# Optimization experiments

Measured on AMD Instinct MI355X. Metric: run time of the kernel, lower is better.

## Reference

```python
import jax, jax.numpy as jnp
import numpy as np

N = 2048            # num nodes
AVG_DEG = 16
E0 = N * AVG_DEG    # random edges; self-loops appended -> E = E0 + N
IN_FEATS = 256
H = 16              # num_heads
HS = 32             # hidden_size (forced by linear001 = Linear(32,16))
D = HS // H         # head_dim = 2
EPS = 1e-5


def gat_conv(x, src, dst, W, al, ar, b):
    # DGL-style GATConv: x [N,F] -> [N,H,D]
    feat = (x @ W).reshape(N, H, D)                      # [N,H,D]
    el = (feat * al[None]).sum(-1)                       # [N,H] (src term)
    er = (feat * ar[None]).sum(-1)                       # [N,H] (dst term)
    e = jax.nn.leaky_relu(el[src] + er[dst], 0.2)        # [E,H]
    m = jax.ops.segment_max(e, dst, num_segments=N)      # segment softmax over incoming edges
    ex = jnp.exp(e - m[dst])
    s = jax.ops.segment_sum(ex, dst, num_segments=N)
    alpha = ex / s[dst]                                  # [E,H]
    out = jax.ops.segment_sum(alpha[:, :, None] * feat[src], dst, num_segments=N)
    return out + b.reshape(1, H, D)


def setup_inputs() -> dict:
    key = jax.random.key(0)
    ks = jax.random.split(key, 40)
    rn = lambda k, s, sc=0.1: (jax.random.normal(k, s, jnp.float32) * sc)
    loops = jnp.arange(N, dtype=jnp.int32)
    src = jnp.concatenate([jax.random.randint(ks[0], (E0,), 0, N, jnp.int32), loops])
    dst = jnp.concatenate([jax.random.randint(ks[1], (E0,), 0, N, jnp.int32), loops])
    inp = {
        'features': jax.random.normal(ks[2], (N, IN_FEATS), jnp.float32),
        'src': src, 'dst': dst,
        # GATConv 1
        'W1': rn(ks[3], (IN_FEATS, HS)), 'al1': rn(ks[4], (H, D)), 'ar1': rn(ks[5], (H, D)), 'bg1': rn(ks[6], (HS,)),
        # GATConv 2
        'W2': rn(ks[7], (HS, HS)), 'al2': rn(ks[8], (H, D)), 'ar2': rn(ks[9], (H, D)), 'bg2': rn(ks[10], (HS,)),
        # dense MHA projections
        'qw': rn(ks[11], (HS, HS)), 'qb': rn(ks[12], (HS,)),
        'kw': rn(ks[13], (HS, HS)), 'kb': rn(ks[14], (HS,)),
        'vw': rn(ks[15], (HS, HS)), 'vb': rn(ks[16], (HS,)),
        'ow': rn(ks[17], (HS, HS)), 'ob': rn(ks[18], (HS,)),
        # batchnorm affine
        'bn_g': jnp.ones((HS,), jnp.float32), 'bn_b': jnp.zeros((HS,), jnp.float32),
        # mlp
        'm1w': rn(ks[19], (HS, HS // 2)), 'm1b': rn(ks[20], (HS // 2,)),
        'm2w': rn(ks[21], (HS // 2, HS)), 'm2b': rn(ks[22], (HS,)),
        # scoring head
        'w001': rn(ks[23], (32, 16)), 'b001': rn(ks[24], (16,)),
        'w01': rn(ks[25], (16, 8)), 'b01': rn(ks[26], (8,)),
        'w1': rn(ks[27], (8, 4)), 'b1': rn(ks[28], (4,)),
        'w2': rn(ks[29], (4, 1)), 'b2': rn(ks[30], (1,)),
    }
    return inp


def reference(features, src, dst, W1, al1, ar1, bg1, W2, al2, ar2, bg2,
              qw, qb, kw, kb, vw, vb, ow, ob, bn_g, bn_b,
              m1w, m1b, m2w, m2b, w001, b001, w01, b01, w1, b1, w2, b2):
    h = gat_conv(features, src, dst, W1, al1, ar1, bg1).reshape(N, HS)
    h = gat_conv(h, src, dst, W2, al2, ar2, bg2).reshape(N, HS)
    # manual dense multi-head attention across all nodes
    Q = (h @ qw + qb).reshape(N, H, D)
    K = (h @ kw + kb).reshape(N, H, D)
    V = (h @ vw + vb).reshape(N, H, D)
    scores = jnp.einsum('nhd,mhd->hnm', Q, K) / jnp.sqrt(jnp.float32(D))  # [H,N,N]
    attn = jax.nn.softmax(scores, axis=-1)
    ao = jnp.einsum('hnm,mhd->nhd', attn, V).reshape(N, HS)
    ao = ao @ ow + ob
    # BatchNorm1d (training mode: batch stats, biased variance)
    mu = ao.mean(0)
    var = ao.var(0)
    ao = (ao - mu) / jnp.sqrt(var + EPS) * bn_g + bn_b
    # MLP
    ao = jax.nn.relu(ao @ m1w + m1b)
    ao = jax.nn.relu(ao @ m2w + m2b)
    # scoring head
    z = jax.nn.leaky_relu(ao @ w001 + b001, 0.01)
    z = jax.nn.leaky_relu(z @ w01 + b01, 0.01)
    z = jax.nn.leaky_relu(z @ w1 + b1, 0.01)
    return jax.nn.sigmoid(z @ w2 + b2)  # [N,1]
```

## Files before the change

### kernel.cpp

```cpp
#include <hip/hip_runtime.h>
#include <math.h>

#define NN 2048
#define NH 16
#define HSZ 32
#define INF_ 256
#define CAP 64

__global__ void __launch_bounds__(256) k_front(
    const float* __restrict__ x, const float* __restrict__ W1,
    const float* __restrict__ al, const float* __restrict__ ar,
    const int* __restrict__ src, const int* __restrict__ dst, int E,
    int* __restrict__ cnt, int* __restrict__ adj, float* __restrict__ feat,
    float* __restrict__ el, float* __restrict__ er) {
    __shared__ float xs[4][INF_];
    __shared__ float row[4][HSZ];
    const int tid = threadIdx.x;
    const int gtid = blockIdx.x * 256 + tid;
    const int lane = tid & 63, wsl = tid >> 6, gw = gtid >> 6;
    const int j = lane & 31, half = lane >> 5;

    if (gtid < E) {
        int d = dst[gtid];
        int pos = atomicAdd(&cnt[d], 1);
        if (pos < CAP) adj[d * CAP + pos] = src[gtid];
    }

    int n = gw;
    ((float4*)xs[wsl])[lane] = ((const float4*)(x + (size_t)n * INF_))[lane];
    __syncthreads();
    float acc = 0.f;
    const float4* x4 = (const float4*)xs[wsl];
#pragma unroll
    for (int k4 = 0; k4 < 32; ++k4) {
        float4 xq = x4[half * 32 + k4];
        int k = half * 128 + 4 * k4;
        acc += xq.x * W1[(k + 0) * HSZ + j];
        acc += xq.y * W1[(k + 1) * HSZ + j];
        acc += xq.z * W1[(k + 2) * HSZ + j];
        acc += xq.w * W1[(k + 3) * HSZ + j];
    }
    acc += __shfl_xor(acc, 32);
    if (half == 0) {
        feat[n * HSZ + j] = acc;
        row[wsl][j] = acc;
    }
    __syncthreads();
    if (lane < NH) {
        el[n * NH + lane] =
            row[wsl][2 * lane] * al[2 * lane] + row[wsl][2 * lane + 1] * al[2 * lane + 1];
    } else if (lane < 2 * NH) {
        int h = lane - NH;
        er[n * NH + h] =
            row[wsl][2 * h] * ar[2 * h] + row[wsl][2 * h + 1] * ar[2 * h + 1];
    }
}

__global__ void __launch_bounds__(256) k_seg_gat2(
    const int* __restrict__ cnt, const int* __restrict__ adj,
    const float* __restrict__ el, const float* __restrict__ er,
    const float* __restrict__ feat, const float* __restrict__ bg,
    const float* __restrict__ W2, const float* __restrict__ al2,
    const float* __restrict__ ar2, float* __restrict__ feat2,
    float* __restrict__ el2, float* __restrict__ er2) {
    __shared__ float row[4][HSZ];
    __shared__ float xv[4][HSZ];
    const int tid = threadIdx.x;
    const int gtid = blockIdx.x * 256 + tid;
    const int lane = tid & 63, wsl = tid >> 6, gw = gtid >> 6;
    const int j = lane & 31, half = lane >> 5;
    int n = gw;
    int h = lane >> 2, q = lane & 3;
    int deg = cnt[n]; deg = deg < CAP ? deg : CAP;
    int base = n * CAP;
    float erv = er[n * NH + h];
    float sum = 0.f, a0 = 0.f, a1 = 0.f;
    for (int jj = q; jj < deg; jj += 4) {
        int s = adj[base + jj];
        float v = el[s * NH + h] + erv;
        v = v > 0.f ? v : 0.2f * v;
        float ex = __expf(v);
        float2 f = ((const float2*)feat)[s * NH + h];
        sum += ex; a0 += ex * f.x; a1 += ex * f.y;
    }
    sum += __shfl_xor(sum, 1); a0 += __shfl_xor(a0, 1); a1 += __shfl_xor(a1, 1);
    sum += __shfl_xor(sum, 2); a0 += __shfl_xor(a0, 2); a1 += __shfl_xor(a1, 2);
    if (q == 0) {
        float rs = 1.f / sum;
        row[wsl][2 * h]     = a0 * rs + bg[2 * h];
        row[wsl][2 * h + 1] = a1 * rs + bg[2 * h + 1];
    }
    __syncthreads();
    float acc = 0.f;
#pragma unroll
    for (int c = half * 16; c < half * 16 + 16; ++c) acc += row[wsl][c] * W2[c * HSZ + j];
    acc += __shfl_xor(acc, 32);
    if (half == 0) {
        feat2[n * HSZ + j] = acc;
        xv[wsl][j] = acc;
    }
    __syncthreads();
    if (lane < NH) {
        el2[n * NH + lane] =
            xv[wsl][2 * lane] * al2[2 * lane] + xv[wsl][2 * lane + 1] * al2[2 * lane + 1];
    } else if (lane < 2 * NH) {
        int h2 = lane - NH;
        er2[n * NH + h2] =
            xv[wsl][2 * h2] * ar2[2 * h2] + xv[wsl][2 * h2 + 1] * ar2[2 * h2 + 1];
    }
}

__global__ void __launch_bounds__(256) k_seg_qkv(
    const int* __restrict__ cnt, const int* __restrict__ adj,
    const float* __restrict__ el2, const float* __restrict__ er2,
    const float* __restrict__ feat2, const float* __restrict__ bg,
    const float* __restrict__ qw, const float* __restrict__ qb,
    const float* __restrict__ kw, const float* __restrict__ kb,
    const float* __restrict__ vw, const float* __restrict__ vb,
    float* __restrict__ Q, float* __restrict__ KV) {
    __shared__ float row[4][HSZ];
    const int tid = threadIdx.x;
    const int gtid = blockIdx.x * 256 + tid;
    const int lane = tid & 63, wsl = tid >> 6, gw = gtid >> 6;
    const int j = lane & 31, half = lane >> 5;
    int n = gw;
    int h = lane >> 2, q = lane & 3;
    int deg = cnt[n]; deg = deg < CAP ? deg : CAP;
    int base = n * CAP;
    float erv = er2[n * NH + h];
    float sum = 0.f, a0 = 0.f, a1 = 0.f;
    for (int jj = q; jj < deg; jj += 4) {
        int s = adj[base + jj];
        float v = el2[s * NH + h] + erv;
        v = v > 0.f ? v : 0.2f * v;
        float ex = __expf(v);
        float2 f = ((const float2*)feat2)[s * NH + h];
        sum += ex; a0 += ex * f.x; a1 += ex * f.y;
    }
    sum += __shfl_xor(sum, 1); a0 += __shfl_xor(a0, 1); a1 += __shfl_xor(a1, 1);
    sum += __shfl_xor(sum, 2); a0 += __shfl_xor(a0, 2); a1 += __shfl_xor(a1, 2);
    if (q == 0) {
        float rs = 1.f / sum;
        row[wsl][2 * h]     = a0 * rs + bg[2 * h];
        row[wsl][2 * h + 1] = a1 * rs + bg[2 * h + 1];
    }
    __syncthreads();
    float qa = 0.f, ka = 0.f, va = 0.f;
#pragma unroll
    for (int c = half * 16; c < half * 16 + 16; ++c) {
        float hv = row[wsl][c];
        qa += hv * qw[c * HSZ + j];
        ka += hv * kw[c * HSZ + j];
        va += hv * vw[c * HSZ + j];
    }
    qa += __shfl_xor(qa, 32);
    ka += __shfl_xor(ka, 32);
    va += __shfl_xor(va, 32);
    if (half == 0) {
        const float QS = 0.70710678118654752f * 1.44269504088896340f;
        Q[n * HSZ + j] = (qa + qb[j]) * QS;
        int hh = j >> 1, d = j & 1;
        KV[(hh * NN + n) * 4 + d]     = ka + kb[j];
        KV[(hh * NN + n) * 4 + 2 + d] = va + vb[j];
    }
}

__global__ void __launch_bounds__(256) k_attn16(
    const float* __restrict__ Q, const float* __restrict__ KV,
    float* __restrict__ ao) {
    const int gtid = blockIdx.x * 256 + threadIdx.x;
    const int gw = gtid >> 6;
    const int lane = gtid & 63;
    int hh = gw >> 7;
    int q0 = (gw & 127) * 16;
    const float4* KV4 = (const float4*)KV + hh * NN;
    const float2* Q2 = (const float2*)Q;
    float qx[16], qy[16], sm[16], a0[16], a1[16];
#pragma unroll
    for (int i = 0; i < 16; ++i) {
        float2 qq = Q2[(q0 + i) * NH + hh];
        qx[i] = qq.x; qy[i] = qq.y;
        sm[i] = 0.f; a0[i] = 0.f; a1[i] = 0.f;
    }
#pragma unroll 2
    for (int it = 0; it < NN / 64; ++it) {
        float4 kv = KV4[it * 64 + lane];
#pragma unroll
        for (int i = 0; i < 16; ++i) {
            float pe = exp2f(qx[i] * kv.x + qy[i] * kv.y);
            sm[i] += pe; a0[i] += pe * kv.z; a1[i] += pe * kv.w;
        }
    }
#pragma unroll
    for (int i = 0; i < 16; ++i) {
#pragma unroll
        for (int off = 32; off; off >>= 1) {
            sm[i] += __shfl_xor(sm[i], off);
            a0[i] += __shfl_xor(a0[i], off);
            a1[i] += __shfl_xor(a1[i], off);
        }
        if (lane == 0) {
            float rs = 1.f / sm[i];
            ((float2*)ao)[(q0 + i) * NH + hh] = make_float2(a0[i] * rs, a1[i] * rs);
        }
    }
}

#define M1W 0
#define M2W 512
#define W001 1024
#define W01 1536
#define W1O 1664
#define W2O 1696
#define M1B 1700
#define M2B 1716
#define B001 1748
#define B01 1764
#define B1O 1772
#define B2O 1776
__global__ void __launch_bounds__(256) k_opt(
    const float* __restrict__ ao, const float* __restrict__ ow,
    const float* __restrict__ ob, const float* __restrict__ bn_g,
    const float* __restrict__ bn_b, const float* __restrict__ m1w,
    const float* __restrict__ m1b, const float* __restrict__ m2w,
    const float* __restrict__ m2b, const float* __restrict__ w001,
    const float* __restrict__ b001, const float* __restrict__ w01,
    const float* __restrict__ b01, const float* __restrict__ w1,
    const float* __restrict__ b1, const float* __restrict__ w2,
    const float* __restrict__ b2, float* __restrict__ bnbuf,
    int* __restrict__ done, float* __restrict__ out) {
    __shared__ float w_s[1844];
    __shared__ float ao_s[8][33];
    __shared__ float xr[8][33];
    __shared__ float AB[64];
    __shared__ float yb[8][17];
    __shared__ float zb[8][33];
    __shared__ float ab[8][17];
    __shared__ float bb[8][9];
    __shared__ float cb[8][5];
    const int t = threadIdx.x;
    const int n0 = blockIdx.x * 8;

    w_s[M1W + t] = m1w[t];            w_s[M1W + 256 + t] = m1w[256 + t];
    w_s[M2W + t] = m2w[t];            w_s[M2W + 256 + t] = m2w[256 + t];
    w_s[W001 + t] = w001[t];          w_s[W001 + 256 + t] = w001[256 + t];
    if (t < 128) w_s[W01 + t] = w01[t];
    if (t < 32) { w_s[W1O + t] = w1[t]; w_s[M2B + t] = m2b[t]; }
    if (t < 16) { w_s[M1B + t] = m1b[t]; w_s[B001 + t] = b001[t]; }
    if (t < 8) w_s[B01 + t] = b01[t];
    if (t < 4) { w_s[B1O + t] = b1[t]; w_s[W2O + t] = w2[t]; }
    if (t == 0) w_s[B2O] = b2[0];
    {
        int nl = t >> 5, j = t & 31;
        ao_s[nl][j] = ao[(n0 + nl) * HSZ + j];
    }
    __syncthreads();

    const int nl = t >> 5, j = t & 31;
    {
        float a = ob[j];
#pragma unroll
        for (int c = 0; c < HSZ; ++c) a += ao_s[nl][c] * ow[c * HSZ + j];
        xr[nl][j] = a;
    }
    __syncthreads();
    if (t < HSZ) {
        float s = 0.f, qsum = 0.f;
#pragma unroll
        for (int r = 0; r < 8; ++r) { float v = xr[r][t]; s += v; qsum += v * v; }
        atomicAdd(&bnbuf[t], s);
        atomicAdd(&bnbuf[HSZ + t], qsum);
    }
    __syncthreads();
    if (t == 0) {
        __hip_atomic_fetch_add(done, 1, __ATOMIC_RELEASE, __HIP_MEMORY_SCOPE_AGENT);
        while (__hip_atomic_load(done, __ATOMIC_ACQUIRE, __HIP_MEMORY_SCOPE_AGENT) < 256) {
            __builtin_amdgcn_s_sleep(2);
        }
    }
    __syncthreads();
    if (t < HSZ) {
        const float invN = 1.f / NN;
        float s = __hip_atomic_load(&bnbuf[t], __ATOMIC_RELAXED, __HIP_MEMORY_SCOPE_AGENT);
        float qs = __hip_atomic_load(&bnbuf[HSZ + t], __ATOMIC_RELAXED, __HIP_MEMORY_SCOPE_AGENT);
        float mu = s * invN;
        float var = qs * invN - mu * mu;
        float A = rsqrtf(var + 1e-5f) * bn_g[t];
        AB[t] = A;
        AB[HSZ + t] = bn_b[t] - mu * A;
    }
    __syncthreads();
    xr[nl][j] = xr[nl][j] * AB[j] + AB[HSZ + j];
    __syncthreads();

    const int s5 = j;
    if (s5 < 16) {
        float a = w_s[M1B + s5];
#pragma unroll
        for (int i = 0; i < 32; ++i) a += xr[nl][i] * w_s[M1W + i * 16 + s5];
        yb[nl][s5] = fmaxf(a, 0.f);
    }
    __syncthreads();
    {
        float a = w_s[M2B + s5];
#pragma unroll
        for (int i = 0; i < 16; ++i) a += yb[nl][i] * w_s[M2W + i * 32 + s5];
        zb[nl][s5] = fmaxf(a, 0.f);
    }
    __syncthreads();
    if (s5 < 16) {
        float a = w_s[B001 + s5];
#pragma unroll
        for (int i = 0; i < 32; ++i) a += zb[nl][i] * w_s[W001 + i * 16 + s5];
        ab[nl][s5] = a > 0.f ? a : 0.01f * a;
    }
    __syncthreads();
    if (s5 < 8) {
        float a = w_s[B01 + s5];
#pragma unroll
        for (int i = 0; i < 16; ++i) a += ab[nl][i] * w_s[W01 + i * 8 + s5];
        bb[nl][s5] = a > 0.f ? a : 0.01f * a;
    }
    __syncthreads();
    if (s5 < 4) {
        float a = w_s[B1O + s5];
#pragma unroll
        for (int i = 0; i < 8; ++i) a += bb[nl][i] * w_s[W1O + i * 4 + s5];
        cb[nl][s5] = a > 0.f ? a : 0.01f * a;
    }
    __syncthreads();
    if (s5 == 0) {
        float d = w_s[B2O];
#pragma unroll
        for (int i = 0; i < 4; ++i) d += cb[nl][i] * w_s[W2O + i];
        out[n0 + nl] = 1.f / (1.f + __expf(-d));
    }
}

extern "C" void kernel_launch(void* const* d_in, const int* in_sizes, int n_in,
                              void* d_out, int out_size, void* d_ws, size_t ws_size,
                              hipStream_t stream) {
    const float* features = (const float*)d_in[0];
    const int* src = (const int*)d_in[1];
    const int* dst = (const int*)d_in[2];
    const float* W1 = (const float*)d_in[3];
    const float* al1 = (const float*)d_in[4];
    const float* ar1 = (const float*)d_in[5];
    const float* bg1 = (const float*)d_in[6];
    const float* W2 = (const float*)d_in[7];
    const float* al2 = (const float*)d_in[8];
    const float* ar2 = (const float*)d_in[9];
    const float* bg2 = (const float*)d_in[10];
    const float* qw = (const float*)d_in[11];
    const float* qb = (const float*)d_in[12];
    const float* kw = (const float*)d_in[13];
    const float* kb = (const float*)d_in[14];
    const float* vw = (const float*)d_in[15];
    const float* vb = (const float*)d_in[16];
    const float* ow = (const float*)d_in[17];
    const float* ob = (const float*)d_in[18];
    const float* bn_g = (const float*)d_in[19];
    const float* bn_b = (const float*)d_in[20];
    const float* m1w = (const float*)d_in[21];
    const float* m1b = (const float*)d_in[22];
    const float* m2w = (const float*)d_in[23];
    const float* m2b = (const float*)d_in[24];
    const float* w001 = (const float*)d_in[25];
    const float* b001 = (const float*)d_in[26];
    const float* w01 = (const float*)d_in[27];
    const float* b01 = (const float*)d_in[28];
    const float* w1 = (const float*)d_in[29];
    const float* b1 = (const float*)d_in[30];
    const float* w2 = (const float*)d_in[31];
    const float* b2 = (const float*)d_in[32];

    int E = in_sizes[1];

    float* wsp = (float*)d_ws;
    float* feat = wsp;
    float* el = feat + NN * HSZ;
    float* er = el + NN * NH;
    float* feat2 = er + NN * NH;
    float* el2 = feat2 + NN * HSZ;
    float* er2 = el2 + NN * NH;
    float* Q = er2 + NN * NH;
    float* KV = Q + NN * HSZ;
    float* ao = KV + NN * HSZ * 2;
    float* bnbuf = ao + NN * HSZ;
    int* done = (int*)(bnbuf + 64);
    int* cnt = done + 16;
    int* adj = cnt + NN;

    dim3 b256(256);
    hipMemsetAsync(bnbuf, 0, (64 + 16 + NN) * sizeof(float), stream);

    k_front<<<512, b256, 0, stream>>>(features, W1, al1, ar1, src, dst, E,
                                      cnt, adj, feat, el, er);
    k_seg_gat2<<<512, b256, 0, stream>>>(cnt, adj, el, er, feat, bg1,
                                         W2, al2, ar2, feat2, el2, er2);
    k_seg_qkv<<<512, b256, 0, stream>>>(cnt, adj, el2, er2, feat2, bg2,
                                        qw, qb, kw, kb, vw, vb, Q, KV);
    k_attn16<<<512, b256, 0, stream>>>(Q, KV, ao);
    k_opt<<<256, b256, 0, stream>>>(ao, ow, ob, bn_g, bn_b, m1w, m1b, m2w, m2b,
                                    w001, b001, w01, b01, w1, b1, w2, b2,
                                    bnbuf, done, (float*)d_out);
}
```

Baseline: 188.9 us.

## Fuse five pipeline kernels into two persistent kernels with grid barriers

Merges front/GAT2 into one kernel and QKV/attention/MLP-head into another, separating stages with atomic-counter grid barriers instead of kernel launches. The MLP/BN tail now uses 512 blocks of 4 nodes each instead of 256 blocks of 8. This removes launch gaps and per-kernel drain between stages. In exchange, correctness relies on all 512 blocks being co-resident (launch_bounds 256,2), and the spin barriers add polling and synchronisation latency.

```diff
diff --git a/kernel.cpp b/kernel.cpp
--- a/kernel.cpp
+++ b/kernel.cpp
@@ -6,202 +6,121 @@
 #define HSZ 32
 #define INF_ 256
 #define CAP 64
-
-__global__ void __launch_bounds__(256) k_front(
+#define NBLK 512
+
+__device__ __forceinline__ void gbar_acq(int* ctr, int nb) {
+    __syncthreads();
+    if (threadIdx.x == 0) {
+        __hip_atomic_fetch_add(ctr, 1, __ATOMIC_RELEASE, __HIP_MEMORY_SCOPE_AGENT);
+        while (__hip_atomic_load(ctr, __ATOMIC_ACQUIRE, __HIP_MEMORY_SCOPE_AGENT) < nb)
+            __builtin_amdgcn_s_sleep(4);
+    }
+    __syncthreads();
+}
+__device__ __forceinline__ void gbar_rlx(int* ctr, int nb) {
+    __syncthreads();
+    if (threadIdx.x == 0) {
+        __hip_atomic_fetch_add(ctr, 1, __ATOMIC_RELAXED, __HIP_MEMORY_SCOPE_AGENT);
+        while (__hip_atomic_load(ctr, __ATOMIC_RELAXED, __HIP_MEMORY_SCOPE_AGENT) < nb)
+            __builtin_amdgcn_s_sleep(4);
+    }
+    __syncthreads();
+}
+
+__global__ void __launch_bounds__(256, 2) k_A(
     const float* __restrict__ x, const float* __restrict__ W1,
-    const float* __restrict__ al, const float* __restrict__ ar,
+    const float* __restrict__ al1, const float* __restrict__ ar1,
     const int* __restrict__ src, const int* __restrict__ dst, int E,
     int* __restrict__ cnt, int* __restrict__ adj, float* __restrict__ feat,
-    float* __restrict__ el, float* __restrict__ er) {
+    float* __restrict__ el, float* __restrict__ er,
+    const float* __restrict__ bg1, const float* __restrict__ W2,
+    const float* __restrict__ al2, const float* __restrict__ ar2,
+    float* __restrict__ feat2, float* __restrict__ el2, float* __restrict__ er2,
+    int* __restrict__ bars) {
     __shared__ float xs[4][INF_];
-    __shared__ float row[4][HSZ];
-    const int tid = threadIdx.x;
-    const int gtid = blockIdx.x * 256 + tid;
-    const int lane = tid & 63, wsl = tid >> 6, gw = gtid >> 6;
-    const int j = lane & 31, half = lane >> 5;
-
-    if (gtid < E) {
-        int d = dst[gtid];
-        int pos = atomicAdd(&cnt[d], 1);
-        if (pos < CAP) adj[d * CAP + pos] = src[gtid];
-    }
-
-    int n = gw;
-    ((float4*)xs[wsl])[lane] = ((const float4*)(x + (size_t)n * INF_))[lane];
-    __syncthreads();
-    float acc = 0.f;
-    const float4* x4 = (const float4*)xs[wsl];
-#pragma unroll
-    for (int k4 = 0; k4 < 32; ++k4) {
-        float4 xq = x4[half * 32 + k4];
-        int k = half * 128 + 4 * k4;
-        acc += xq.x * W1[(k + 0) * HSZ + j];
-        acc += xq.y * W1[(k + 1) * HSZ + j];
-        acc += xq.z * W1[(k + 2) * HSZ + j];
-        acc += xq.w * W1[(k + 3) * HSZ + j];
-    }
-    acc += __shfl_xor(acc, 32);
-    if (half == 0) {
-        feat[n * HSZ + j] = acc;
-        row[wsl][j] = acc;
-    }
-    __syncthreads();
-    if (lane < NH) {
-        el[n * NH + lane] =
-            row[wsl][2 * lane] * al[2 * lane] + row[wsl][2 * lane + 1] * al[2 * lane + 1];
-    } else if (lane < 2 * NH) {
-        int h = lane - NH;
-        er[n * NH + h] =
-            row[wsl][2 * h] * ar[2 * h] + row[wsl][2 * h + 1] * ar[2 * h + 1];
-    }
-}
-
-__global__ void __launch_bounds__(256) k_seg_gat2(
-    const int* __restrict__ cnt, const int* __restrict__ adj,
-    const float* __restrict__ el, const float* __restrict__ er,
-    const float* __restrict__ feat, const float* __restrict__ bg,
-    const float* __restrict__ W2, const float* __restrict__ al2,
-    const float* __restrict__ ar2, float* __restrict__ feat2,
-    float* __restrict__ el2, float* __restrict__ er2) {
     __shared__ float row[4][HSZ];
     __shared__ float xv[4][HSZ];
     const int tid = threadIdx.x;
     const int gtid = blockIdx.x * 256 + tid;
     const int lane = tid & 63, wsl = tid >> 6, gw = gtid >> 6;
     const int j = lane & 31, half = lane >> 5;
-    int n = gw;
-    int h = lane >> 2, q = lane & 3;
-    int deg = cnt[n]; deg = deg < CAP ? deg : CAP;
-    int base = n * CAP;
-    float erv = er[n * NH + h];
-    float sum = 0.f, a0 = 0.f, a1 = 0.f;
-    for (int jj = q; jj < deg; jj += 4) {
-        int s = adj[base + jj];
-        float v = el[s * NH + h] + erv;
-        v = v > 0.f ? v : 0.2f * v;
-        float ex = __expf(v);
-        float2 f = ((const float2*)feat)[s * NH + h];
-        sum += ex; a0 += ex * f.x; a1 += ex * f.y;
-    }
-    sum += __shfl_xor(sum, 1); a0 += __shfl_xor(a0, 1); a1 += __shfl_xor(a1, 1);
-    sum += __shfl_xor(sum, 2); a0 += __shfl_xor(a0, 2); a1 += __shfl_xor(a1, 2);
-    if (q == 0) {
-        float rs = 1.f / sum;
-        row[wsl][2 * h]     = a0 * rs + bg[2 * h];
-        row[wsl][2 * h + 1] = a1 * rs + bg[2 * h + 1];
-    }
-    __syncthreads();
-    float acc = 0.f;
-#pragma unroll
-    for (int c = half * 16; c < half * 16 + 16; ++c) acc += row[wsl][c] * W2[c * HSZ + j];
-    acc += __shfl_xor(acc, 32);
-    if (half == 0) {
-        feat2[n * HSZ + j] = acc;
-        xv[wsl][j] = acc;
-    }
-    __syncthreads();
-    if (lane < NH) {
-        el2[n * NH + lane] =
-            xv[wsl][2 * lane] * al2[2 * lane] + xv[wsl][2 * lane + 1] * al2[2 * lane + 1];
-    } else if (lane < 2 * NH) {
-        int h2 = lane - NH;
-        er2[n * NH + h2] =
-            xv[wsl][2 * h2] * ar2[2 * h2] + xv[wsl][2 * h2 + 1] * ar2[2 * h2 + 1];
-    }
-}
-
-__global__ void __launch_bounds__(256) k_seg_qkv(
-    const int* __restrict__ cnt, const int* __restrict__ adj,
-    const float* __restrict__ el2, const float* __restrict__ er2,
-    const float* __restrict__ feat2, const float* __restrict__ bg,
-    const float* __restrict__ qw, const float* __restrict__ qb,
-    const float* __restrict__ kw, const float* __restrict__ kb,
-    const float* __restrict__ vw, const float* __restrict__ vb,
-    float* __restrict__ Q, float* __restrict__ KV) {
-    __shared__ float row[4][HSZ];
-    const int tid = threadIdx.x;
-    const int gtid = blockIdx.x * 256 + tid;
-    const int lane = tid & 63, wsl = tid >> 6, gw = gtid >> 6;
-    const int j = lane & 31, half = lane >> 5;
-    int n = gw;
-    int h = lane >> 2, q = lane & 3;
-    int deg = cnt[n]; deg = deg < CAP ? deg : CAP;
-    int base = n * CAP;
-    float erv = er2[n * NH + h];
-    float sum = 0.f, a0 = 0.f, a1 = 0.f;
-    for (int jj = q; jj < deg; jj += 4) {
-        int s = adj[base + jj];
-        float v = el2[s * NH + h] + erv;
-        v = v > 0.f ? v : 0.2f * v;
-        float ex = __expf(v);
-        float2 f = ((const float2*)feat2)[s * NH + h];
-        sum += ex; a0 += ex * f.x; a1 += ex * f.y;
-    }
-    sum += __shfl_xor(sum, 1); a0 += __shfl_xor(a0, 1); a1 += __shfl_xor(a1, 1);
-    sum += __shfl_xor(sum, 2); a0 += __shfl_xor(a0, 2); a1 += __shfl_xor(a1, 2);
-    if (q == 0) {
-        float rs = 1.f / sum;
-        row[wsl][2 * h]     = a0 * rs + bg[2 * h];
-        row[wsl][2 * h + 1] = a1 * rs + bg[2 * h + 1];
-    }
-    __syncthreads();
-    float qa = 0.f, ka = 0.f, va = 0.f;
-#pragma unroll
-    for (int c = half * 16; c < half * 16 + 16; ++c) {
-        float hv = row[wsl][c];
-        qa += hv * qw[c * HSZ + j];
-        ka += hv * kw[c * HSZ + j];
-        va += hv * vw[c * HSZ + j];
-    }
-    qa += __shfl_xor(qa, 32);
-    ka += __shfl_xor(ka, 32);
-    va += __shfl_xor(va, 32);
-    if (half == 0) {
-        const float QS = 0.70710678118654752f * 1.44269504088896340f;
-        Q[n * HSZ + j] = (qa + qb[j]) * QS;
-        int hh = j >> 1, d = j & 1;
-        KV[(hh * NN + n) * 4 + d]     = ka + kb[j];
-        KV[(hh * NN + n) * 4 + 2 + d] = va + vb[j];
-    }
-}
-
-__global__ void __launch_bounds__(256) k_attn16(
-    const float* __restrict__ Q, const float* __restrict__ KV,
-    float* __restrict__ ao) {
-    const int gtid = blockIdx.x * 256 + threadIdx.x;
-    const int gw = gtid >> 6;
-    const int lane = gtid & 63;
-    int hh = gw >> 7;
-    int q0 = (gw & 127) * 16;
-    const float4* KV4 = (const float4*)KV + hh * NN;
-    const float2* Q2 = (const float2*)Q;
-    float qx[16], qy[16], sm[16], a0[16], a1[16];
-#pragma unroll
-    for (int i = 0; i < 16; ++i) {
-        float2 qq = Q2[(q0 + i) * NH + hh];
-        qx[i] = qq.x; qy[i] = qq.y;
-        sm[i] = 0.f; a0[i] = 0.f; a1[i] = 0.f;
-    }
-#pragma unroll 2
-    for (int it = 0; it < NN / 64; ++it) {
-        float4 kv = KV4[it * 64 + lane];
-#pragma unroll
-        for (int i = 0; i < 16; ++i) {
-            float pe = exp2f(qx[i] * kv.x + qy[i] * kv.y);
-            sm[i] += pe; a0[i] += pe * kv.z; a1[i] += pe * kv.w;
-        }
-    }
-#pragma unroll
-    for (int i = 0; i < 16; ++i) {
-#pragma unroll
-        for (int off = 32; off; off >>= 1) {
-            sm[i] += __shfl_xor(sm[i], off);
-            a0[i] += __shfl_xor(a0[i], off);
-            a1[i] += __shfl_xor(a1[i], off);
-        }
-        if (lane == 0) {
-            float rs = 1.f / sm[i];
-            ((float2*)ao)[(q0 + i) * NH + hh] = make_float2(a0[i] * rs, a1[i] * rs);
+    const int n = gw;
+
+    if (gtid < E) {
+        int d = dst[gtid];
+        int pos = atomicAdd(&cnt[d], 1);
+        if (pos < CAP) adj[d * CAP + pos] = src[gtid];
+    }
+    ((float4*)xs[wsl])[lane] = ((const float4*)(x + (size_t)n * INF_))[lane];
+    __syncthreads();
+    {
+        float acc = 0.f;
+        const float4* x4 = (const float4*)xs[wsl];
+#pragma unroll
+        for (int k4 = 0; k4 < 32; ++k4) {
+            float4 xq = x4[half * 32 + k4];
+            int k = half * 128 + 4 * k4;
+            acc += xq.x * W1[(k + 0) * HSZ + j];
+            acc += xq.y * W1[(k + 1) * HSZ + j];
+            acc += xq.z * W1[(k + 2) * HSZ + j];
+            acc += xq.w * W1[(k + 3) * HSZ + j];
+        }
+        acc += __shfl_xor(acc, 32);
+        if (half == 0) {
+            feat[n * HSZ + j] = acc;
+            row[wsl][j] = acc;
+        }
+        __syncthreads();
+        if (lane < NH) {
+            el[n * NH + lane] =
+                row[wsl][2 * lane] * al1[2 * lane] + row[wsl][2 * lane + 1] * al1[2 * lane + 1];
+        } else if (lane < 2 * NH) {
+            int h = lane - NH;
+            er[n * NH + h] =
+                row[wsl][2 * h] * ar1[2 * h] + row[wsl][2 * h + 1] * ar1[2 * h + 1];
+        }
+    }
+
+    gbar_acq(&bars[0], NBLK);
+
+    {
+        int h = lane >> 2, q = lane & 3;
+        int deg = cnt[n]; deg = deg < CAP ? deg : CAP;
+        int base = n * CAP;
+        float erv = er[n * NH + h];
+        float sum = 0.f, a0 = 0.f, a1 = 0.f;
+        for (int jj = q; jj < deg; jj += 4) {
+            int s = adj[base + jj];
+            float v = el[s * NH + h] + erv;
+            v = v > 0.f ? v : 0.2f * v;
+            float ex = __expf(v);
+            float2 f = ((const float2*)feat)[s * NH + h];
+            sum += ex; a0 += ex * f.x; a1 += ex * f.y;
+        }
+        sum += __shfl_xor(sum, 1); a0 += __shfl_xor(a0, 1); a1 += __shfl_xor(a1, 1);
+        sum += __shfl_xor(sum, 2); a0 += __shfl_xor(a0, 2); a1 += __shfl_xor(a1, 2);
+        if (q == 0) {
+            float rs = 1.f / sum;
+            row[wsl][2 * h]     = a0 * rs + bg1[2 * h];
+            row[wsl][2 * h + 1] = a1 * rs + bg1[2 * h + 1];
+        }
+        __syncthreads();
+        float acc = 0.f;
+#pragma unroll
+        for (int c = half * 16; c < half * 16 + 16; ++c) acc += row[wsl][c] * W2[c * HSZ + j];
+        acc += __shfl_xor(acc, 32);
+        if (half == 0) {
+            feat2[n * HSZ + j] = acc;
+            xv[wsl][j] = acc;
+        }
+        __syncthreads();
+        if (lane < NH) {
+            el2[n * NH + lane] =
+                xv[wsl][2 * lane] * al2[2 * lane] + xv[wsl][2 * lane + 1] * al2[2 * lane + 1];
+        } else if (lane < 2 * NH) {
+            int h2 = lane - NH;
+            er2[n * NH + h2] =
+                xv[wsl][2 * h2] * ar2[2 * h2] + xv[wsl][2 * h2 + 1] * ar2[2 * h2 + 1];
         }
     }
 }
@@ -218,121 +137,204 @@
 #define B01 1764
 #define B1O 1772
 #define B2O 1776
-__global__ void __launch_bounds__(256) k_opt(
-    const float* __restrict__ ao, const float* __restrict__ ow,
-    const float* __restrict__ ob, const float* __restrict__ bn_g,
-    const float* __restrict__ bn_b, const float* __restrict__ m1w,
-    const float* __restrict__ m1b, const float* __restrict__ m2w,
-    const float* __restrict__ m2b, const float* __restrict__ w001,
-    const float* __restrict__ b001, const float* __restrict__ w01,
-    const float* __restrict__ b01, const float* __restrict__ w1,
-    const float* __restrict__ b1, const float* __restrict__ w2,
-    const float* __restrict__ b2, float* __restrict__ bnbuf,
-    int* __restrict__ done, float* __restrict__ out) {
+__global__ void __launch_bounds__(256, 2) k_B(
+    const int* __restrict__ cnt, const int* __restrict__ adj,
+    const float* __restrict__ el2, const float* __restrict__ er2,
+    const float* __restrict__ feat2, const float* __restrict__ bg2,
+    const float* __restrict__ qw, const float* __restrict__ qb,
+    const float* __restrict__ kw, const float* __restrict__ kb,
+    const float* __restrict__ vw, const float* __restrict__ vb,
+    float* __restrict__ Q, float* __restrict__ KV, float* __restrict__ ao,
+    const float* __restrict__ ow, const float* __restrict__ ob,
+    const float* __restrict__ bn_g, const float* __restrict__ bn_b,
+    const float* __restrict__ m1w, const float* __restrict__ m1b,
+    const float* __restrict__ m2w, const float* __restrict__ m2b,
+    const float* __restrict__ w001, const float* __restrict__ b001,
+    const float* __restrict__ w01, const float* __restrict__ b01,
+    const float* __restrict__ w1, const float* __restrict__ b1,
+    const float* __restrict__ w2, const float* __restrict__ b2,
+    float* __restrict__ bnbuf, int* __restrict__ bars, float* __restrict__ out) {
+    __shared__ float row[4][HSZ];
     __shared__ float w_s[1844];
-    __shared__ float ao_s[8][33];
-    __shared__ float xr[8][33];
+    __shared__ float ao_s[4][33];
+    __shared__ float xr[4][33];
     __shared__ float AB[64];
-    __shared__ float yb[8][17];
-    __shared__ float zb[8][33];
-    __shared__ float ab[8][17];
-    __shared__ float bb[8][9];
-    __shared__ float cb[8][5];
-    const int t = threadIdx.x;
-    const int n0 = blockIdx.x * 8;
-
-    w_s[M1W + t] = m1w[t];            w_s[M1W + 256 + t] = m1w[256 + t];
-    w_s[M2W + t] = m2w[t];            w_s[M2W + 256 + t] = m2w[256 + t];
-    w_s[W001 + t] = w001[t];          w_s[W001 + 256 + t] = w001[256 + t];
-    if (t < 128) w_s[W01 + t] = w01[t];
-    if (t < 32) { w_s[W1O + t] = w1[t]; w_s[M2B + t] = m2b[t]; }
-    if (t < 16) { w_s[M1B + t] = m1b[t]; w_s[B001 + t] = b001[t]; }
-    if (t < 8) w_s[B01 + t] = b01[t];
-    if (t < 4) { w_s[B1O + t] = b1[t]; w_s[W2O + t] = w2[t]; }
-    if (t == 0) w_s[B2O] = b2[0];
+    __shared__ float yb[4][17];
+    __shared__ float zb[4][33];
+    __shared__ float ab_[4][17];
+    __shared__ float bb_[4][9];
+    __shared__ float cb_[4][5];
+    const int tid = threadIdx.x;
+    const int gtid = blockIdx.x * 256 + tid;
+    const int lane = tid & 63, wsl = tid >> 6, gw = gtid >> 6;
+    const int j = lane & 31, half = lane >> 5;
+
     {
-        int nl = t >> 5, j = t & 31;
-        ao_s[nl][j] = ao[(n0 + nl) * HSZ + j];
-    }
-    __syncthreads();
-
-    const int nl = t >> 5, j = t & 31;
+        const int n = gw;
+        int h = lane >> 2, q = lane & 3;
+        int deg = cnt[n]; deg = deg < CAP ? deg : CAP;
+        int base = n * CAP;
+        float erv = er2[n * NH + h];
+        float sum = 0.f, a0 = 0.f, a1 = 0.f;
+        for (int jj = q; jj < deg; jj += 4) {
+            int s = adj[base + jj];
+            float v = el2[s * NH + h] + erv;
+            v = v > 0.f ? v : 0.2f * v;
+            float ex = __expf(v);
+            float2 f = ((const float2*)feat2)[s * NH + h];
+            sum += ex; a0 += ex * f.x; a1 += ex * f.y;
+        }
+        sum += __shfl_xor(sum, 1); a0 += __shfl_xor(a0, 1); a1 += __shfl_xor(a1, 1);
+        sum += __shfl_xor(sum, 2); a0 += __shfl_xor(a0, 2); a1 += __shfl_xor(a1, 2);
+        if (q == 0) {
+            float rs = 1.f / sum;
+            row[wsl][2 * h]     = a0 * rs + bg2[2 * h];
+            row[wsl][2 * h + 1] = a1 * rs + bg2[2 * h + 1];
+        }
+        __syncthreads();
+        float qa = 0.f, ka = 0.f, va = 0.f;
+#pragma unroll
+        for (int c = half * 16; c < half * 16 + 16; ++c) {
+            float hv = row[wsl][c];
+            qa += hv * qw[c * HSZ + j];
+            ka += hv * kw[c * HSZ + j];
+            va += hv * vw[c * HSZ + j];
+        }
+        qa += __shfl_xor(qa, 32);
+        ka += __shfl_xor(ka, 32);
+        va += __shfl_xor(va, 32);
+        if (half == 0) {
+            const float QS = 0.70710678118654752f * 1.44269504088896340f;
+            Q[n * HSZ + j] = (qa + qb[j]) * QS;
+            int hh = j >> 1, d = j & 1;
+            KV[(hh * NN + n) * 4 + d]     = ka + kb[j];
+            KV[(hh * NN + n) * 4 + 2 + d] = va + vb[j];
+        }
+    }
+
+    gbar_acq(&bars[1], NBLK);
+
     {
-        float a = ob[j];
-#pragma unroll
-        for (int c = 0; c < HSZ; ++c) a += ao_s[nl][c] * ow[c * HSZ + j];
-        xr[nl][j] = a;
-    }
-    __syncthreads();
-    if (t < HSZ) {
+        int hh = gw >> 7;
+        int q0 = (gw & 127) * 16;
+        const float4* KV4 = (const float4*)KV + hh * NN;
+        const float2* Q2 = (const float2*)Q;
+        float qx[16], qy[16], sm[16], a0[16], a1[16];
+#pragma unroll
+        for (int i = 0; i < 16; ++i) {
+            float2 qq = Q2[(q0 + i) * NH + hh];
+            qx[i] = qq.x; qy[i] = qq.y;
+            sm[i] = 0.f; a0[i] = 0.f; a1[i] = 0.f;
+        }
+#pragma unroll 2
+        for (int it = 0; it < NN / 64; ++it) {
+            float4 kv = KV4[it * 64 + lane];
+#pragma unroll
+            for (int i = 0; i < 16; ++i) {
+                float pe = exp2f(qx[i] * kv.x + qy[i] * kv.y);
+                sm[i] += pe; a0[i] += pe * kv.z; a1[i] += pe * kv.w;
+            }
+        }
+#pragma unroll
+        for (int i = 0; i < 16; ++i) {
+#pragma unroll
+            for (int off = 32; off; off >>= 1) {
+                sm[i] += __shfl_xor(sm[i], off);
+                a0[i] += __shfl_xor(a0[i], off);
+                a1[i] += __shfl_xor(a1[i], off);
+            }
+            if (lane == 0) {
+                float rs = 1.f / sm[i];
+                ((float2*)ao)[(q0 + i) * NH + hh] = make_float2(a0[i] * rs, a1[i] * rs);
+            }
+        }
+    }
+
+    w_s[M1W + tid] = m1w[tid];            w_s[M1W + 256 + tid] = m1w[256 + tid];
+    w_s[M2W + tid] = m2w[tid];            w_s[M2W + 256 + tid] = m2w[256 + tid];
+    w_s[W001 + tid] = w001[tid];          w_s[W001 + 256 + tid] = w001[256 + tid];
+    if (tid < 128) w_s[W01 + tid] = w01[tid];
+    if (tid < 32) { w_s[W1O + tid] = w1[tid]; w_s[M2B + tid] = m2b[tid]; }
+    if (tid < 16) { w_s[M1B + tid] = m1b[tid]; w_s[B001 + tid] = b001[tid]; }
+    if (tid < 8) w_s[B01 + tid] = b01[tid];
+    if (tid < 4) { w_s[B1O + tid] = b1[tid]; w_s[W2O + tid] = w2[tid]; }
+    if (tid == 0) w_s[B2O] = b2[0];
+
+    gbar_acq(&bars[2], NBLK);
+
+    const int n0 = blockIdx.x * 4;
+    const int nl = tid >> 5, s5 = tid & 31;
+    if (tid < 128) ao_s[nl][s5] = ao[(n0 + nl) * HSZ + s5];
+    __syncthreads();
+    if (tid < 128) {
+        float a = ob[s5];
+#pragma unroll
+        for (int c = 0; c < HSZ; ++c) a += ao_s[nl][c] * ow[c * HSZ + s5];
+        xr[nl][s5] = a;
+    }
+    __syncthreads();
+    if (tid < HSZ) {
         float s = 0.f, qsum = 0.f;
 #pragma unroll
-        for (int r = 0; r < 8; ++r) { float v = xr[r][t]; s += v; qsum += v * v; }
-        atomicAdd(&bnbuf[t], s);
-        atomicAdd(&bnbuf[HSZ + t], qsum);
-    }
-    __syncthreads();
-    if (t == 0) {
-        __hip_atomic_fetch_add(done, 1, __ATOMIC_RELEASE, __HIP_MEMORY_SCOPE_AGENT);
-        while (__hip_atomic_load(done, __ATOMIC_ACQUIRE, __HIP_MEMORY_SCOPE_AGENT) < 256) {
-            __builtin_amdgcn_s_sleep(2);
-        }
-    }
-    __syncthreads();
-    if (t < HSZ) {
+        for (int r = 0; r < 4; ++r) { float v = xr[r][tid]; s += v; qsum += v * v; }
+        atomicAdd(&bnbuf[tid], s);
+        atomicAdd(&bnbuf[HSZ + tid], qsum);
+    }
+
+    gbar_rlx(&bars[3], NBLK);
+
+    if (tid < HSZ) {
         const float invN = 1.f / NN;
-        float s = __hip_atomic_load(&bnbuf[t], __ATOMIC_RELAXED, __HIP_MEMORY_SCOPE_AGENT);
-        float qs = __hip_atomic_load(&bnbuf[HSZ + t], __ATOMIC_RELAXED, __HIP_MEMORY_SCOPE_AGENT);
+        float s = __hip_atomic_load(&bnbuf[tid], __ATOMIC_RELAXED, __HIP_MEMORY_SCOPE_AGENT);
+        float qs = __hip_atomic_load(&bnbuf[HSZ + tid], __ATOMIC_RELAXED, __HIP_MEMORY_SCOPE_AGENT);
         float mu = s * invN;
         float var = qs * invN - mu * mu;
-        float A = rsqrtf(var + 1e-5f) * bn_g[t];
-        AB[t] = A;
-        AB[HSZ + t] = bn_b[t] - mu * A;
-    }
-    __syncthreads();
-    xr[nl][j] = xr[nl][j] * AB[j] + AB[HSZ + j];
-    __syncthreads();
-
-    const int s5 = j;
-    if (s5 < 16) {
+        float A = rsqrtf(var + 1e-5f) * bn_g[tid];
+        AB[tid] = A;
+        AB[HSZ + tid] = bn_b[tid] - mu * A;
+    }
+    __syncthreads();
+    if (tid < 128) xr[nl][s5] = xr[nl][s5] * AB[s5] + AB[HSZ + s5];
+    __syncthreads();
+    if (tid < 128 && s5 < 16) {
         float a = w_s[M1B + s5];
 #pragma unroll
         for (int i = 0; i < 32; ++i) a += xr[nl][i] * w_s[M1W + i * 16 + s5];
         yb[nl][s5] = fmaxf(a, 0.f);
     }
     __syncthreads();
-    {
+    if (tid < 128) {
         float a = w_s[M2B + s5];
 #pragma unroll
         for (int i = 0; i < 16; ++i) a += yb[nl][i] * w_s[M2W + i * 32 + s5];
         zb[nl][s5] = fmaxf(a, 0.f);
     }
     __syncthreads();
-    if (s5 < 16) {
+    if (tid < 128 && s5 < 16) {
         float a = w_s[B001 + s5];
 #pragma unroll
         for (int i = 0; i < 32; ++i) a += zb[nl][i] * w_s[W001 + i * 16 + s5];
-        ab[nl][s5] = a > 0.f ? a : 0.01f * a;
-    }
-    __syncthreads();
-    if (s5 < 8) {
+        ab_[nl][s5] = a > 0.f ? a : 0.01f * a;
+    }
+    __syncthreads();
+    if (tid < 128 && s5 < 8) {
         float a = w_s[B01 + s5];
 #pragma unroll
-        for (int i = 0; i < 16; ++i) a += ab[nl][i] * w_s[W01 + i * 8 + s5];
-        bb[nl][s5] = a > 0.f ? a : 0.01f * a;
-    }
-    __syncthreads();
-    if (s5 < 4) {
+        for (int i = 0; i < 16; ++i) a += ab_[nl][i] * w_s[W01 + i * 8 + s5];
+        bb_[nl][s5] = a > 0.f ? a : 0.01f * a;
+    }
+    __syncthreads();
+    if (tid < 128 && s5 < 4) {
         float a = w_s[B1O + s5];
 #pragma unroll
-        for (int i = 0; i < 8; ++i) a += bb[nl][i] * w_s[W1O + i * 4 + s5];
-        cb[nl][s5] = a > 0.f ? a : 0.01f * a;
-    }
-    __syncthreads();
-    if (s5 == 0) {
+        for (int i = 0; i < 8; ++i) a += bb_[nl][i] * w_s[W1O + i * 4 + s5];
+        cb_[nl][s5] = a > 0.f ? a : 0.01f * a;
+    }
+    __syncthreads();
+    if (tid < 128 && s5 == 0) {
         float d = w_s[B2O];
 #pragma unroll
-        for (int i = 0; i < 4; ++i) d += cb[nl][i] * w_s[W2O + i];
+        for (int i = 0; i < 4; ++i) d += cb_[nl][i] * w_s[W2O + i];
         out[n0 + nl] = 1.f / (1.f + __expf(-d));
     }
 }
@@ -387,21 +389,18 @@
     float* KV = Q + NN * HSZ;
     float* ao = KV + NN * HSZ * 2;
     float* bnbuf = ao + NN * HSZ;
-    int* done = (int*)(bnbuf + 64);
-    int* cnt = done + 16;
+    int* bars = (int*)(bnbuf + 64);
+    int* cnt = bars + 16;
     int* adj = cnt + NN;
 
-    dim3 b256(256);
     hipMemsetAsync(bnbuf, 0, (64 + 16 + NN) * sizeof(float), stream);
 
-    k_front<<<512, b256, 0, stream>>>(features, W1, al1, ar1, src, dst, E,
-                                      cnt, adj, feat, el, er);
-    k_seg_gat2<<<512, b256, 0, stream>>>(cnt, adj, el, er, feat, bg1,
-                                         W2, al2, ar2, feat2, el2, er2);
-    k_seg_qkv<<<512, b256, 0, stream>>>(cnt, adj, el2, er2, feat2, bg2,
-                                        qw, qb, kw, kb, vw, vb, Q, KV);
-    k_attn16<<<512, b256, 0, stream>>>(Q, KV, ao);
-    k_opt<<<256, b256, 0, stream>>>(ao, ow, ob, bn_g, bn_b, m1w, m1b, m2w, m2b,
-                                    w001, b001, w01, b01, w1, b1, w2, b2,
-                                    bnbuf, done, (float*)d_out);
+    k_A<<<NBLK, dim3(256), 0, stream>>>(features, W1, al1, ar1, src, dst, E,
+                                        cnt, adj, feat, el, er,
+                                        bg1, W2, al2, ar2, feat2, el2, er2, bars);
+    k_B<<<NBLK, dim3(256), 0, stream>>>(cnt, adj, el2, er2, feat2, bg2,
+                                        qw, qb, kw, kb, vw, vb, Q, KV, ao,
+                                        ow, ob, bn_g, bn_b, m1w, m1b, m2w, m2b,
+                                        w001, b001, w01, b01, w1, b1, w2, b2,
+                                        bnbuf, bars, (float*)d_out);
 }
```

Result: slower. 328.4 us (+73.9%).
